# Performance work log

Hardware: AMD Instinct MI355X
Metric: run time of the kernel (lower is better)

Reference implementation:

```python
import jax, jax.numpy as jnp
import numpy as np

B, IN_CAPS, OUT_CAPS, DIM_CAPS, ITERS = 128, 1152, 16, 16, 3


def setup_inputs() -> dict:
    key = jax.random.key(0)
    kx, kw = jax.random.split(key)
    x = jax.random.normal(kx, (B, IN_CAPS, 8), dtype=jnp.float32)
    W = jax.random.normal(kw, (1, IN_CAPS, OUT_CAPS, DIM_CAPS, 8), dtype=jnp.float32)
    return {"x": x, "W": W}


def _squash(t):
    # squash over last axis (dim=3), exactly as the torch module
    sq = jnp.sum(t * t, axis=3, keepdims=True)
    scale = sq / (1.0 + sq)
    unit = t / jnp.sqrt(sq + 1e-8)
    return scale * unit


def reference(x, W):
    # u_hat: [B, in, out, dim] = W [1,in,out,dim,8] contracted with x [B,in,8]
    u_hat = jnp.einsum('iodk,bik->biod', W[0], x)
    b = jnp.zeros((x.shape[0], IN_CAPS, OUT_CAPS, 1), dtype=x.dtype)
    v = None
    for i in range(ITERS):
        c = jax.nn.softmax(b, axis=2)
        # note: after iter 0, b/c are [B,in,out,out]; elementwise with u_hat
        # requires out_caps == dim_caps (faithful to the original module)
        s = jnp.sum(c * u_hat, axis=1, keepdims=True)  # [B,1,out,dim]
        v = _squash(s)
        if i < ITERS - 1:
            # agreement: [B,in,out,out]
            agreement = jnp.matmul(u_hat, jnp.swapaxes(v, 2, 3))
            b = b + agreement
    return jnp.squeeze(v, axis=1)  # [B, out, dim]
```

## Files before the change

### kernel.cpp

```cpp
#include <hip/hip_runtime.h>

typedef _Float16 h4 __attribute__((ext_vector_type(4)));
typedef float    f4 __attribute__((ext_vector_type(4)));

#define N_B   128
#define N_IN  1152
#define ICH   12
#define NCH   96
#define BSPL  8
#define BCH   16
#define TPW   3

#define WSWZ_SZ  (N_IN * 64 * 32 * 4)
#define VSUM_OFF (WSWZ_SZ)
#define VSUM_SZ  (N_B * 256 * 4)
#define SBUF_OFF (VSUM_OFF + VSUM_SZ)
#define SBUF_SZ  (N_B * 256 * 4)

__global__ __launch_bounds__(256) void k_setup(const float* __restrict__ W,
                                               float* __restrict__ Wswz,
                                               float* __restrict__ Vsum,
                                               float* __restrict__ S) {
    int t = blockIdx.x * 256 + threadIdx.x;
    if (t < N_B * 256) { Vsum[t] = 0.f; S[t] = 0.f; }
    int i = t >> 6, lane = t & 63;
    if (i < N_IN) {
        int o = lane & 15, jq = lane >> 4;
        const f4* src = (const f4*)(W + ((size_t)((i * 16 + o) * 16 + jq * 4) * 8));
        f4* dst = (f4*)(Wswz + (size_t)t * 32);
#pragma unroll
        for (int q = 0; q < 8; q++) dst[q] = src[q];
    }
}

__global__ __launch_bounds__(256, 3) void k_route(const float* __restrict__ x,
                                                  const float* __restrict__ Wswz,
                                                  const float* __restrict__ Vsum,
                                                  float* __restrict__ S,
                                                  int iter) {
    __shared__ _Float16 vsh[BCH][16][20];
    __shared__ _Float16 vsl[BCH][16][20];
    __shared__ float red[4][256];

    const int bx   = blockIdx.x;
    const int c    = bx >> 3;
    const int spl  = bx & 7;
    const int i0   = c * ICH;
    const int b0   = spl * BCH;
    const int tid  = threadIdx.x;
    const int w    = tid >> 6;
    const int lane = tid & 63;
    const int lo16 = lane & 15;
    const int jq   = lane >> 4;

    f4 wreg[TPW][8];
    {
        const f4* wp = (const f4*)Wswz + ((size_t)(i0 + w * TPW) * 64 + lane) * 8;
#pragma unroll
        for (int t3 = 0; t3 < TPW; t3++)
#pragma unroll
            for (int q = 0; q < 8; q++) wreg[t3][q] = wp[t3 * 512 + q];
    }

    if (iter) {
#pragma unroll
        for (int e = 0; e < BCH; e++) {
            float v = Vsum[(size_t)(b0 + e) * 256 + tid];
            _Float16 h = (_Float16)v;
            _Float16 l = (_Float16)(v - (float)h);
            vsh[e][tid >> 4][tid & 15] = h;
            vsl[e][tid >> 4][tid & 15] = l;
        }
    }
    __syncthreads();

    h4 idf;
#pragma unroll
    for (int t = 0; t < 4; t++) idf[t] = (_Float16)((jq * 4 + t == lo16) ? 1.0f : 0.0f);

    for (int bb = 0; bb < BCH; bb++) {
        const int b = b0 + bb;
        float sacc[4] = {0.f, 0.f, 0.f, 0.f};
        h4 bh, bl;
        if (iter) {
#pragma unroll
            for (int t = 0; t < 4; t++) {
                bh[t] = vsh[bb][lo16][jq * 4 + t];
                bl[t] = vsl[bb][lo16][jq * 4 + t];
            }
        }
#pragma unroll
        for (int t3 = 0; t3 < TPW; t3++) {
            const int i = i0 + w * TPW + t3;
            const float* xp = x + ((size_t)b * N_IN + i) * 8;
            f4 xa = *((const f4*)xp);
            f4 xb = *((const f4*)xp + 1);
            float u[4];
#pragma unroll
            for (int t = 0; t < 4; t++) {
                float a = 0.f;
#pragma unroll
                for (int k = 0; k < 4; k++) a = fmaf(wreg[t3][2 * t][k], xa[k], a);
#pragma unroll
                for (int k = 0; k < 4; k++) a = fmaf(wreg[t3][2 * t + 1][k], xb[k], a);
                u[t] = a;
            }
            if (iter == 0) {
#pragma unroll
                for (int t = 0; t < 4; t++) sacc[t] = fmaf(u[t], 0.0625f, sacc[t]);
            } else {
                h4 uh, ul;
#pragma unroll
                for (int t = 0; t < 4; t++) {
                    _Float16 h = (_Float16)u[t];
                    uh[t] = h;
                    ul[t] = (_Float16)(u[t] - (float)h);
                }
                f4 z = {0.f, 0.f, 0.f, 0.f};
                f4 L = __builtin_amdgcn_mfma_f32_16x16x16f16(uh, bh, z, 0, 0, 0);
                L = __builtin_amdgcn_mfma_f32_16x16x16f16(ul, bh, L, 0, 0, 0);
                L = __builtin_amdgcn_mfma_f32_16x16x16f16(uh, bl, L, 0, 0, 0);
                f4 ud = __builtin_amdgcn_mfma_f32_16x16x16f16(uh, idf, z, 0, 0, 0);
                ud = __builtin_amdgcn_mfma_f32_16x16x16f16(ul, idf, ud, 0, 0, 0);
                float p[4]; float zs = 0.f;
#pragma unroll
                for (int t = 0; t < 4; t++) { p[t] = __expf(L[t]); zs += p[t]; }
                zs += __shfl_xor(zs, 16);
                zs += __shfl_xor(zs, 32);
                float rin = __builtin_amdgcn_rcpf(zs);
#pragma unroll
                for (int t = 0; t < 4; t++) sacc[t] = fmaf(p[t] * rin, ud[t], sacc[t]);
            }
        }
        if (iter == 0) {
#pragma unroll
            for (int t = 0; t < 4; t++) red[w][lo16 * 16 + jq * 4 + t] = sacc[t];
        } else {
#pragma unroll
            for (int t = 0; t < 4; t++) red[w][(jq * 4 + t) * 16 + lo16] = sacc[t];
        }
        __syncthreads();
        float val = (red[0][tid] + red[1][tid]) + (red[2][tid] + red[3][tid]);
        atomicAdd(S + (size_t)b * 256 + tid, val);
        __syncthreads();
    }
}

__global__ __launch_bounds__(256) void k_squash(float* __restrict__ S,
                                                float* __restrict__ Vsum,
                                                float* __restrict__ out) {
    int b = blockIdx.x, tid = threadIdx.x;
    size_t idx = (size_t)b * 256 + tid;
    float s = S[idx];
    S[idx] = 0.f;
    float sq = s * s;
    sq += __shfl_xor(sq, 1);
    sq += __shfl_xor(sq, 2);
    sq += __shfl_xor(sq, 4);
    sq += __shfl_xor(sq, 8);
    float scale = sq * __builtin_amdgcn_rcpf(1.f + sq);
    float rs = __builtin_amdgcn_rsqf(sq + 1e-8f);
    float v = s * scale * rs;
    out[idx] = v;
    Vsum[idx] += v;
}

extern "C" void kernel_launch(void* const* d_in, const int* in_sizes, int n_in,
                              void* d_out, int out_size, void* d_ws, size_t ws_size,
                              hipStream_t stream) {
    (void)in_sizes; (void)n_in; (void)out_size; (void)ws_size;
    const float* x = (const float*)d_in[0];
    const float* W = (const float*)d_in[1];
    float* out  = (float*)d_out;
    char*  ws   = (char*)d_ws;
    float* Wswz = (float*)ws;
    float* Vsum = (float*)(ws + VSUM_OFF);
    float* S    = (float*)(ws + SBUF_OFF);

    k_setup<<<288, 256, 0, stream>>>(W, Wswz, Vsum, S);
    for (int it = 0; it < 3; it++) {
        k_route<<<NCH * BSPL, 256, 0, stream>>>(x, Wswz, Vsum, S, it);
        k_squash<<<N_B, 256, 0, stream>>>(S, Vsum, out);
    }
}
```

Before: 230.2 us.

## Replace global atomics with per-chunk partial sums and deterministic reduction

Drops the W swizzle setup kernel and reads W directly in its natural layout. The routing kernel now accumulates into per-block shared memory with LDS atomics and writes per-chunk partial sums, which a templated reduce-squash kernel sums across 72 chunks. Iteration 0 gets its own simpler kernel, and Vsum is read directly from global memory instead of being staged in LDS. This removes global float atomics and the zeroing passes. In exchange it adds a large partial-sum buffer that must be written and re-read each iteration, plus uncoalesced W loads.

Result: slower. 479.9 us (+108.5%).

```diff
diff --git a/kernel.cpp b/kernel.cpp
--- a/kernel.cpp
+++ b/kernel.cpp
@@ -5,110 +5,120 @@
 
 #define N_B   128
 #define N_IN  1152
-#define ICH   12
-#define NCH   96
+#define TPW   2
+#define NSTG  2
+#define ICH   (TPW * 4 * NSTG)
+#define NCH   (N_IN / ICH)
 #define BSPL  8
-#define BCH   16
-#define TPW   3
+#define BCH   (N_B / BSPL)
 
-#define WSWZ_SZ  (N_IN * 64 * 32 * 4)
-#define VSUM_OFF (WSWZ_SZ)
-#define VSUM_SZ  (N_B * 256 * 4)
-#define SBUF_OFF (VSUM_OFF + VSUM_SZ)
-#define SBUF_SZ  (N_B * 256 * 4)
+#define SPART_SZ ((size_t)NCH * N_B * 256 * 4)
 
-__global__ __launch_bounds__(256) void k_setup(const float* __restrict__ W,
-                                               float* __restrict__ Wswz,
-                                               float* __restrict__ Vsum,
-                                               float* __restrict__ S) {
-    int t = blockIdx.x * 256 + threadIdx.x;
-    if (t < N_B * 256) { Vsum[t] = 0.f; S[t] = 0.f; }
-    int i = t >> 6, lane = t & 63;
-    if (i < N_IN) {
-        int o = lane & 15, jq = lane >> 4;
-        const f4* src = (const f4*)(W + ((size_t)((i * 16 + o) * 16 + jq * 4) * 8));
-        f4* dst = (f4*)(Wswz + (size_t)t * 32);
+
+__global__ __launch_bounds__(256, 3) void k_route0(const float* __restrict__ x,
+                                                   const float* __restrict__ W,
+                                                   float* __restrict__ Spart) {
+    __shared__ float sblk[BCH * 256];
+    const int c = blockIdx.x, spl = blockIdx.y;
+    const int b0 = spl * BCH;
+    const int tid = threadIdx.x, w = tid >> 6, lane = tid & 63;
+    const int lo = lane & 15, hi = lane >> 4;
+
 #pragma unroll
-        for (int q = 0; q < 8; q++) dst[q] = src[q];
+    for (int r = 0; r < BCH; r++) sblk[r * 256 + tid] = 0.f;
+    __syncthreads();
+
+    for (int stg = 0; stg < NSTG; stg++) {
+        const int ibase = c * ICH + stg * (TPW * 4) + w * TPW;
+        f4 wreg[TPW][8];
+#pragma unroll
+        for (int t3 = 0; t3 < TPW; t3++) {
+            const f4* wp = (const f4*)(W + (size_t)(((ibase + t3) * 16 + lo) * 16 + hi * 4) * 8);
+#pragma unroll
+            for (int q = 0; q < 8; q++) wreg[t3][q] = wp[q];
+        }
+        for (int bbi = 0; bbi < BCH; bbi++) {
+            const int bb = (bbi + w * 4) & (BCH - 1);
+            const int b = b0 + bb;
+            float sacc[4] = {0.f, 0.f, 0.f, 0.f};
+#pragma unroll
+            for (int t3 = 0; t3 < TPW; t3++) {
+                const f4* xp = (const f4*)(x + ((size_t)b * N_IN + ibase + t3) * 8);
+                f4 xa = xp[0], xb = xp[1];
+#pragma unroll
+                for (int t = 0; t < 4; t++) {
+                    float a = 0.f;
+#pragma unroll
+                    for (int k = 0; k < 4; k++) a = fmaf(wreg[t3][2 * t][k], xa[k], a);
+#pragma unroll
+                    for (int k = 0; k < 4; k++) a = fmaf(wreg[t3][2 * t + 1][k], xb[k], a);
+                    sacc[t] += a;
+                }
+            }
+#pragma unroll
+            for (int t = 0; t < 4; t++)
+                atomicAdd(&sblk[bb * 256 + t * 64 + lane], sacc[t] * 0.0625f);
+        }
     }
+    __syncthreads();
+#pragma unroll
+    for (int r = 0; r < BCH; r++)
+        Spart[((size_t)c * N_B + b0 + r) * 256 + tid] = sblk[r * 256 + tid];
 }
 
 __global__ __launch_bounds__(256, 3) void k_route(const float* __restrict__ x,
-                                                  const float* __restrict__ Wswz,
+                                                  const float* __restrict__ W,
                                                   const float* __restrict__ Vsum,
-                                                  float* __restrict__ S,
-                                                  int iter) {
-    __shared__ _Float16 vsh[BCH][16][20];
-    __shared__ _Float16 vsl[BCH][16][20];
-    __shared__ float red[4][256];
+                                                  float* __restrict__ Spart) {
+    __shared__ float sblk[BCH * 256];
+    const int c = blockIdx.x, spl = blockIdx.y;
+    const int b0 = spl * BCH;
+    const int tid = threadIdx.x, w = tid >> 6, lane = tid & 63;
+    const int lo = lane & 15, hi = lane >> 4;
 
-    const int bx   = blockIdx.x;
-    const int c    = bx >> 3;
-    const int spl  = bx & 7;
-    const int i0   = c * ICH;
-    const int b0   = spl * BCH;
-    const int tid  = threadIdx.x;
-    const int w    = tid >> 6;
-    const int lane = tid & 63;
-    const int lo16 = lane & 15;
-    const int jq   = lane >> 4;
-
-    f4 wreg[TPW][8];
-    {
-        const f4* wp = (const f4*)Wswz + ((size_t)(i0 + w * TPW) * 64 + lane) * 8;
 #pragma unroll
-        for (int t3 = 0; t3 < TPW; t3++)
-#pragma unroll
-            for (int q = 0; q < 8; q++) wreg[t3][q] = wp[t3 * 512 + q];
-    }
-
-    if (iter) {
-#pragma unroll
-        for (int e = 0; e < BCH; e++) {
-            float v = Vsum[(size_t)(b0 + e) * 256 + tid];
-            _Float16 h = (_Float16)v;
-            _Float16 l = (_Float16)(v - (float)h);
-            vsh[e][tid >> 4][tid & 15] = h;
-            vsl[e][tid >> 4][tid & 15] = l;
-        }
-    }
+    for (int r = 0; r < BCH; r++) sblk[r * 256 + tid] = 0.f;
     __syncthreads();
 
     h4 idf;
 #pragma unroll
-    for (int t = 0; t < 4; t++) idf[t] = (_Float16)((jq * 4 + t == lo16) ? 1.0f : 0.0f);
+    for (int t = 0; t < 4; t++) idf[t] = (_Float16)((hi * 4 + t == lo) ? 1.f : 0.f);
 
-    for (int bb = 0; bb < BCH; bb++) {
-        const int b = b0 + bb;
-        float sacc[4] = {0.f, 0.f, 0.f, 0.f};
-        h4 bh, bl;
-        if (iter) {
+    for (int stg = 0; stg < NSTG; stg++) {
+        const int ibase = c * ICH + stg * (TPW * 4) + w * TPW;
+        f4 wreg[TPW][8];
+#pragma unroll
+        for (int t3 = 0; t3 < TPW; t3++) {
+            const f4* wp = (const f4*)(W + (size_t)(((ibase + t3) * 16 + lo) * 16 + hi * 4) * 8);
+#pragma unroll
+            for (int q = 0; q < 8; q++) wreg[t3][q] = wp[q];
+        }
+        for (int bbi = 0; bbi < BCH; bbi++) {
+            const int bb = (bbi + w * 4) & (BCH - 1);
+            const int b = b0 + bb;
+            f4 vv = *(const f4*)(Vsum + ((size_t)b * 256 + lo * 16 + hi * 4));
+            h4 bh, bl;
 #pragma unroll
             for (int t = 0; t < 4; t++) {
-                bh[t] = vsh[bb][lo16][jq * 4 + t];
-                bl[t] = vsl[bb][lo16][jq * 4 + t];
+                _Float16 h = (_Float16)vv[t];
+                bh[t] = h;
+                bl[t] = (_Float16)(vv[t] - (float)h);
             }
-        }
+            float sacc[4] = {0.f, 0.f, 0.f, 0.f};
 #pragma unroll
-        for (int t3 = 0; t3 < TPW; t3++) {
-            const int i = i0 + w * TPW + t3;
-            const float* xp = x + ((size_t)b * N_IN + i) * 8;
-            f4 xa = *((const f4*)xp);
-            f4 xb = *((const f4*)xp + 1);
-            float u[4];
+            for (int t3 = 0; t3 < TPW; t3++) {
+                const f4* xp = (const f4*)(x + ((size_t)b * N_IN + ibase + t3) * 8);
+                f4 xa = xp[0], xb = xp[1];
+                float u[4];
 #pragma unroll
-            for (int t = 0; t < 4; t++) {
-                float a = 0.f;
+                for (int t = 0; t < 4; t++) {
+                    float a = 0.f;
 #pragma unroll
-                for (int k = 0; k < 4; k++) a = fmaf(wreg[t3][2 * t][k], xa[k], a);
+                    for (int k = 0; k < 4; k++) a = fmaf(wreg[t3][2 * t][k], xa[k], a);
 #pragma unroll
-                for (int k = 0; k < 4; k++) a = fmaf(wreg[t3][2 * t + 1][k], xb[k], a);
-                u[t] = a;
-            }
-            if (iter == 0) {
-#pragma unroll
-                for (int t = 0; t < 4; t++) sacc[t] = fmaf(u[t], 0.0625f, sacc[t]);
-            } else {
+                    for (int k = 0; k < 4; k++) a = fmaf(wreg[t3][2 * t + 1][k], xb[k], a);
+                    u[t] = a;
+                }
                 h4 uh, ul;
 #pragma unroll
                 for (int t = 0; t < 4; t++) {
@@ -122,7 +132,7 @@
                 L = __builtin_amdgcn_mfma_f32_16x16x16f16(uh, bl, L, 0, 0, 0);
                 f4 ud = __builtin_amdgcn_mfma_f32_16x16x16f16(uh, idf, z, 0, 0, 0);
                 ud = __builtin_amdgcn_mfma_f32_16x16x16f16(ul, idf, ud, 0, 0, 0);
-                float p[4]; float zs = 0.f;
+                float p[4], zs = 0.f;
 #pragma unroll
                 for (int t = 0; t < 4; t++) { p[t] = __expf(L[t]); zs += p[t]; }
                 zs += __shfl_xor(zs, 16);
@@ -131,38 +141,39 @@
 #pragma unroll
                 for (int t = 0; t < 4; t++) sacc[t] = fmaf(p[t] * rin, ud[t], sacc[t]);
             }
+#pragma unroll
+            for (int t = 0; t < 4; t++)
+                atomicAdd(&sblk[bb * 256 + t * 64 + lane], sacc[t]);
         }
-        if (iter == 0) {
+    }
+    __syncthreads();
 #pragma unroll
-            for (int t = 0; t < 4; t++) red[w][lo16 * 16 + jq * 4 + t] = sacc[t];
-        } else {
-#pragma unroll
-            for (int t = 0; t < 4; t++) red[w][(jq * 4 + t) * 16 + lo16] = sacc[t];
-        }
-        __syncthreads();
-        float val = (red[0][tid] + red[1][tid]) + (red[2][tid] + red[3][tid]);
-        atomicAdd(S + (size_t)b * 256 + tid, val);
-        __syncthreads();
-    }
+    for (int r = 0; r < BCH; r++)
+        Spart[((size_t)c * N_B + b0 + r) * 256 + tid] = sblk[r * 256 + tid];
 }
 
-__global__ __launch_bounds__(256) void k_squash(float* __restrict__ S,
-                                                float* __restrict__ Vsum,
-                                                float* __restrict__ out) {
-    int b = blockIdx.x, tid = threadIdx.x;
-    size_t idx = (size_t)b * 256 + tid;
-    float s = S[idx];
-    S[idx] = 0.f;
+template <int MODE>
+__global__ __launch_bounds__(256) void k_redsq(const float* __restrict__ Spart,
+                                               float* __restrict__ Vsum,
+                                               float* __restrict__ out) {
+    const int b = blockIdx.x, tid = threadIdx.x;
+    const int o = tid >> 4, d = tid & 15;
+    const int q = (MODE == 0) ? ((d & 3) * 64 + (d >> 2) * 16 + o)
+                              : ((o & 3) * 64 + (o >> 2) * 16 + d);
+    float s = 0.f;
+#pragma unroll 8
+    for (int cc = 0; cc < NCH; cc++) s += Spart[((size_t)cc * N_B + b) * 256 + q];
     float sq = s * s;
     sq += __shfl_xor(sq, 1);
     sq += __shfl_xor(sq, 2);
     sq += __shfl_xor(sq, 4);
     sq += __shfl_xor(sq, 8);
     float scale = sq * __builtin_amdgcn_rcpf(1.f + sq);
-    float rs = __builtin_amdgcn_rsqf(sq + 1e-8f);
-    float v = s * scale * rs;
-    out[idx] = v;
-    Vsum[idx] += v;
+    float v = s * scale * __builtin_amdgcn_rsqf(sq + 1e-8f);
+    size_t idx = (size_t)b * 256 + tid;
+    if (MODE == 0)      Vsum[idx] = v;
+    else if (MODE == 1) Vsum[idx] += v;
+    else                out[idx] = v;
 }
 
 extern "C" void kernel_launch(void* const* d_in, const int* in_sizes, int n_in,
@@ -171,15 +182,15 @@
     (void)in_sizes; (void)n_in; (void)out_size; (void)ws_size;
     const float* x = (const float*)d_in[0];
     const float* W = (const float*)d_in[1];
-    float* out  = (float*)d_out;
-    char*  ws   = (char*)d_ws;
-    float* Wswz = (float*)ws;
-    float* Vsum = (float*)(ws + VSUM_OFF);
-    float* S    = (float*)(ws + SBUF_OFF);
+    float* out   = (float*)d_out;
+    float* Spart = (float*)d_ws;
+    float* Vsum  = (float*)((char*)d_ws + SPART_SZ);
 
-    k_setup<<<288, 256, 0, stream>>>(W, Wswz, Vsum, S);
-    for (int it = 0; it < 3; it++) {
-        k_route<<<NCH * BSPL, 256, 0, stream>>>(x, Wswz, Vsum, S, it);
-        k_squash<<<N_B, 256, 0, stream>>>(S, Vsum, out);
-    }
+    dim3 rg(NCH, BSPL);
+    k_route0<<<rg, 256, 0, stream>>>(x, W, Spart);
+    k_redsq<0><<<N_B, 256, 0, stream>>>(Spart, Vsum, out);
+    k_route<<<rg, 256, 0, stream>>>(x, W, Vsum, Spart);
+    k_redsq<1><<<N_B, 256, 0, stream>>>(Spart, Vsum, out);
+    k_route<<<rg, 256, 0, stream>>>(x, W, Vsum, Spart);
+    k_redsq<2><<<N_B, 256, 0, stream>>>(Spart, Vsum, out);
 }
```
